# Kernel tuning notes

Hardware: AMD Instinct MI355X
Metric: run time of the kernel (lower is better)

Reference implementation:

```python
import jax, jax.numpy as jnp
import numpy as np

B, S, D, H, F = 8, 1024, 512, 8, 2048
EPS = 1e-3  # keras default for BatchNormalization and LayerNormalization


def _layernorm(x, g, b):
    m = jnp.mean(x, axis=-1, keepdims=True)
    v = jnp.var(x, axis=-1, keepdims=True)
    return (x - m) * jax.lax.rsqrt(v + EPS) * g + b


def setup_inputs() -> dict:
    key = jax.random.key(0)
    ks = jax.random.split(key, 16)
    sc = 0.02
    inp = {
        "Q": jax.random.normal(ks[0], (B, S, D), jnp.float32),
        "K": jax.random.normal(ks[1], (B, S, D), jnp.float32),
        "V": jax.random.normal(ks[2], (B, S, D), jnp.float32),
        # per-head QKV projections stacked: [H, D, D]
        "WQ": jax.random.normal(ks[3], (H, D, D), jnp.float32) * sc,
        "bQ": jnp.zeros((H, D), jnp.float32),
        "WK": jax.random.normal(ks[4], (H, D, D), jnp.float32) * sc,
        "bK": jnp.zeros((H, D), jnp.float32),
        "WV": jax.random.normal(ks[5], (H, D, D), jnp.float32) * sc,
        "bV": jnp.zeros((H, D), jnp.float32),
        "Wo": jax.random.normal(ks[6], (H * D, D), jnp.float32) * sc,
        "bo": jnp.zeros((D,), jnp.float32),
        # FeedForward
        "W0": jax.random.normal(ks[7], (D, F), jnp.float32) * sc,
        "b0": jnp.zeros((F,), jnp.float32),
        "g0": jnp.ones((F,), jnp.float32),
        "be0": jnp.zeros((F,), jnp.float32),
        "m0": jnp.zeros((F,), jnp.float32),   # BN moving mean
        "v0": jnp.ones((F,), jnp.float32),    # BN moving var
        "a0": jnp.zeros((S, F), jnp.float32),  # PReLU alpha (keras default shape/init)
        "W1": jax.random.normal(ks[8], (F, F), jnp.float32) * sc,
        "b1": jnp.zeros((F,), jnp.float32),
        "g1": jnp.ones((F,), jnp.float32),
        "be1": jnp.zeros((F,), jnp.float32),
        "m1": jnp.zeros((F,), jnp.float32),
        "v1": jnp.ones((F,), jnp.float32),
        "a1": jnp.zeros((S, F), jnp.float32),
        "W2": jax.random.normal(ks[9], (F, D), jnp.float32) * sc,
        "b2": jnp.zeros((D,), jnp.float32),
        "ln0g": jnp.ones((D,), jnp.float32),
        "ln0b": jnp.zeros((D,), jnp.float32),
        "ln1g": jnp.ones((D,), jnp.float32),
        "ln1b": jnp.zeros((D,), jnp.float32),
    }
    return inp


def reference(Q, K, V, WQ, bQ, WK, bK, WV, bV, Wo, bo,
              W0, b0, g0, be0, m0, v0, a0,
              W1, b1, g1, be1, m1, v1, a1,
              W2, b2, ln0g, ln0b, ln1g, ln1b):
    # ---- MultiHeadAttention (all heads batched) ----
    qh = jnp.einsum('bsd,hde->bhse', Q, WQ) + bQ[None, :, None, :]
    kh = jnp.einsum('bsd,hde->bhse', K, WK) + bK[None, :, None, :]
    vh = jnp.einsum('bsd,hde->bhse', V, WV) + bV[None, :, None, :]
    # NOTE: source scales by 1/dk, not 1/sqrt(dk)
    scores = jnp.einsum('bhse,bhte->bhst', qh, kh) * (1.0 / D)
    attn = jax.nn.softmax(scores, axis=-1)
    ctx = jnp.einsum('bhst,bhte->bhse', attn, vh)        # [B,H,S,D]
    cat = jnp.transpose(ctx, (0, 2, 1, 3)).reshape(B, S, H * D)
    mha = cat @ Wo + bo
    x = _layernorm(Q + mha, ln0g, ln0b)
    # ---- FeedForward (inference: BN uses moving stats, dropout off) ----
    h0 = x @ W0 + b0
    h0 = (h0 - m0) * jax.lax.rsqrt(v0 + EPS) * g0 + be0
    h0 = jnp.where(h0 > 0, h0, a0 * h0)                   # PReLU
    h1 = h0 @ W1 + b1
    h1 = (h1 - m1) * jax.lax.rsqrt(v1 + EPS) * g1 + be1
    h1 = jnp.where(h1 > 0, h1, a1 * h1)
    ff = h1 @ W2 + b2
    return _layernorm(x + ff, ln1g, ln1b)
```

## Files before the change

kernel.cpp:

```cpp
#include <hip/hip_runtime.h>
#include <hip/hip_bf16.h>
#include <cstdint>
#include <cstddef>

#define Sd 1024
#define Dd 512
#define Hd 8
#define Fd 2048
#define Bd 8
#define EPSf 1e-3f

typedef __bf16 bf16x8 __attribute__((ext_vector_type(8)));
typedef float f32x4 __attribute__((ext_vector_type(4)));
typedef __attribute__((address_space(3))) unsigned int lds_u32;
typedef __attribute__((address_space(1))) const unsigned int gl_u32;

#define BM 128
#define BN 128
#define BK 32

enum { EPI_BF16 = 0, EPI_F32 = 1, EPI_BNPRELU = 2, EPI_SCORES = 3, EPI_PV = 4 };

__device__ __forceinline__ void gl_lds16(const void* g, void* l) {
  __builtin_amdgcn_global_load_lds((gl_u32*)g, (lds_u32*)l, 16, 0, 0);
}


#define LGKM(n)                                                  \
  asm volatile("s_waitcnt lgkmcnt(" #n ")" ::: "memory");        \
  __builtin_amdgcn_sched_barrier(0)
#define VMC(n) asm volatile("s_waitcnt vmcnt(" #n ")" ::: "memory")

#define LDA_(dst, dof, xr, mh)                                               \
  _Pragma("unroll") for (int i_ = 0; i_ < 4; ++i_)                           \
      dst[i_] = *(const bf16x8*)(aw + (dof) + (xr) + (mh) * 8192 + i_ * 2048);
#define LDB_(dst, dof, xr)                                                   \
  _Pragma("unroll") for (int i_ = 0; i_ < 4; ++i_)                           \
      dst[i_] = *(const bf16x8*)(bw + (dof) + (xr) + i_ * 2048);
#define MFMAQ(q, av, bv)                                                     \
  __builtin_amdgcn_s_setprio(1);                                             \
  {                                                                          \
    _Pragma("unroll") for (int i_ = 0; i_ < 4; ++i_) {                       \
      _Pragma("unroll") for (int n_ = 0; n_ < 4; ++n_)                       \
          acc[(q) * 4 + i_][n_] = __builtin_amdgcn_mfma_f32_16x16x32_bf16(   \
              av[i_], bv[n_], acc[(q) * 4 + i_][n_], 0, 0, 0);               \
    }                                                                        \
  }                                                                          \
  __builtin_amdgcn_s_setprio(0)

template <int EPI>
__global__ __launch_bounds__(512, 2) void big_gemm(
    const __hip_bfloat16* __restrict__ A_,
    const __hip_bfloat16* __restrict__ B_,
    const float* __restrict__ bias_,
    void* __restrict__ C_, int ldc, int K,
    const float* __restrict__ bn_g, const float* __restrict__ bn_b,
    const float* __restrict__ bn_m, const float* __restrict__ bn_v,
    const float* __restrict__ pa) {
  __shared__ __align__(16) char lds[131072];
  const int tid = threadIdx.x;
  const int gx = gridDim.x;
  const int nwg = gx * gridDim.y;
  const int orig = blockIdx.y * gx + blockIdx.x;
  const int wgid = (orig & 7) * (nwg >> 3) + (orig >> 3);
  const int bx = wgid % gx;
  const int by = wgid / gx;
  const int m0 = by * 256, n0 = bx * 256;

  const int lane = tid & 63;
  const int wid = tid >> 6;
  const int wm = wid >> 2;
  const int wn = wid & 3;
  const int fr = lane & 15;
  const int kg = lane >> 4;

  const int r0 = tid >> 3;
  const int c0 = (tid & 7) ^ (r0 & 7);
  const size_t ldb = (size_t)K * 2;
  const char* Ab = (const char*)A_ + (size_t)(m0 + r0) * ldb + c0 * 16;
  const char* Bb = (const char*)B_ + (size_t)(n0 + r0) * ldb + c0 * 16;

  const int axor0 = (kg ^ (fr & 7)) << 4;
  const int axor1 = ((4 + kg) ^ (fr & 7)) << 4;
  const char* aw = lds + (wm << 14) + fr * 128;
  const char* bw = lds + 32768 + ((wn >> 1) << 14) + ((wn & 1) << 13) + fr * 128;

  auto STG = [&](int nof, int H, int u) {
    char* L = lds + nof + (H << 14) + tid * 16;
    const char* src = ((H < 2) ? Ab : Bb) + (size_t)((H & 1) * 128) * ldb + (size_t)u * 128;
    gl_lds16(src, L);
    gl_lds16(src + 64 * ldb, L + 8192);
  };

  bf16x8 aA[4], aB[4], bA[4], bB[4];
  f32x4 acc[8][4] = {};
  const int NT = K >> 6;

  STG(0, 0, 0); STG(0, 1, 0); STG(0, 2, 0); STG(0, 3, 0);
  STG(65536, 0, 1); STG(65536, 1, 1); STG(65536, 2, 1); STG(65536, 3, 1);
  VMC(8);
  __builtin_amdgcn_s_barrier();
  LDA_(aA, 0, axor0, 0);
  LDB_(bA, 0, axor0);

  for (int u = 0; u < NT; ++u) {
    const int dof = (u & 1) << 16;
    const int nof = dof ^ 65536;
    const bool stg = (u >= 1) & (u + 1 < NT);
    LDA_(aB, dof, axor0, 1);
    if (stg) { STG(nof, 0, u + 1); STG(nof, 1, u + 1); }
    LGKM(4);
    MFMAQ(0, aA, bA);
    LDA_(aA, dof, axor1, 0);
    LDB_(bB, dof, axor1);
    if (stg) { STG(nof, 2, u + 1); STG(nof, 3, u + 1); }
    LGKM(8);
    MFMAQ(1, aB, bA);
    LDA_(aB, dof, axor1, 1);
    LGKM(4);
    MFMAQ(0, aA, bB);
    LGKM(0);
    if (u + 1 < NT) {
      VMC(0);
      __builtin_amdgcn_s_barrier();
      LDA_(aA, nof, axor0, 0);
      LDB_(bA, nof, axor0);
    }
    MFMAQ(1, aB, bB);
  }

  char* C = (char*)C_;
#pragma unroll
  for (int ni = 0; ni < 4; ++ni) {
    const int col = n0 + wn * 64 + ni * 16 + fr;
    float bcol = 0.f, scale = 0.f, shift = 0.f;
    if (EPI != EPI_BF16) bcol = bias_[col];
    if (EPI == EPI_BNPRELU) {
      scale = bn_g[col] * rsqrtf(bn_v[col] + EPSf);
      shift = bn_b[col] - bn_m[col] * scale;
    }
#pragma unroll
    for (int mi = 0; mi < 8; ++mi) {
      const int rb = m0 + wm * 128 + mi * 16 + kg * 4;
#pragma unroll
      for (int j = 0; j < 4; ++j) {
        const int row = rb + j;
        float v = acc[mi][ni][j] + bcol;
        if (EPI == EPI_F32) {
          ((float*)C)[(size_t)row * ldc + col] = v;
        } else if (EPI == EPI_BF16) {
          ((__hip_bfloat16*)C)[(size_t)row * ldc + col] = __float2bfloat16(v);
        } else {
          v = v * scale + shift;
          const float aa = pa[(size_t)(row & (Sd - 1)) * Fd + col];
          v = v > 0.f ? v : aa * v;
          ((__hip_bfloat16*)C)[(size_t)row * ldc + col] = __float2bfloat16(v);
        }
      }
    }
  }
}

template <int EPI>
__global__ __launch_bounds__(256, 2) void bt_gemm(
    const __hip_bfloat16* __restrict__ A_, int lda, size_t sA1, size_t sA2,
    const __hip_bfloat16* __restrict__ B_, int ldb, size_t sB1, size_t sB2,
    const float* __restrict__ bias_, size_t sBi1, size_t sBi2,
    void* __restrict__ C_, int ldc, size_t sC1, size_t sC2,
    int K, float alpha, int zshift,
    const float* __restrict__ bn_g, const float* __restrict__ bn_b,
    const float* __restrict__ bn_m, const float* __restrict__ bn_v,
    const float* __restrict__ pa) {
  __shared__ __hip_bfloat16 As[BM * BK];
  __shared__ __hip_bfloat16 Bs[BN * BK];

  const int tid = threadIdx.x;
  const int z = blockIdx.z;
  const int z1 = z >> zshift;
  const int z2 = z & ((1 << zshift) - 1);
  const int m0 = blockIdx.y * BM;
  const int n0 = blockIdx.x * BN;

  const __hip_bfloat16* A = A_ + (size_t)z1 * sA1 + (size_t)z2 * sA2;
  const __hip_bfloat16* Bt = B_ + (size_t)z1 * sB1 + (size_t)z2 * sB2;
  const float* bi = bias_ ? bias_ + (size_t)z1 * sBi1 + (size_t)z2 * sBi2 : nullptr;

  const int lane = tid & 63;
  const int wv = tid >> 6;
  const int wm = (wv >> 1) * 64;
  const int wn = (wv & 1) * 64;
  const int fr = lane & 15;
  const int kg = lane >> 4;

  const int srow = tid >> 2, sch = tid & 3;
  const size_t ldab = (size_t)lda * 2, ldbb = (size_t)ldb * 2;
  const char* Ap = (const char*)A + (size_t)(m0 + srow) * ldab + sch * 16;
  const char* Ap2 = Ap + 64 * ldab;
  const char* Bp = (const char*)Bt + (size_t)(n0 + srow) * ldbb + sch * 16;
  const char* Bp2 = Bp + 64 * ldbb;
  char* lA = (char*)As + tid * 16;
  char* lB = (char*)Bs + tid * 16;

  f32x4 acc[4][4] = {};

  for (int kt = 0; kt < K; kt += BK) {
    const size_t kb = (size_t)kt * 2;
    gl_lds16(Ap + kb, lA);
    gl_lds16(Ap2 + kb, lA + 4096);
    gl_lds16(Bp + kb, lB);
    gl_lds16(Bp2 + kb, lB + 4096);
    __syncthreads();

    bf16x8 afr[4], bfr[4];
#pragma unroll
    for (int mi = 0; mi < 4; ++mi)
      afr[mi] = *reinterpret_cast<const bf16x8*>(As + (wm + mi * 16 + fr) * BK + kg * 8);
#pragma unroll
    for (int ni = 0; ni < 4; ++ni)
      bfr[ni] = *reinterpret_cast<const bf16x8*>(Bs + (wn + ni * 16 + fr) * BK + kg * 8);
#pragma unroll
    for (int mi = 0; mi < 4; ++mi)
#pragma unroll
      for (int ni = 0; ni < 4; ++ni)
        acc[mi][ni] = __builtin_amdgcn_mfma_f32_16x16x32_bf16(afr[mi], bfr[ni], acc[mi][ni], 0, 0, 0);
    __syncthreads();
  }

  char* C = (char*)C_ + ((size_t)z1 * sC1 + (size_t)z2 * sC2) * ((EPI == EPI_F32) ? 4 : 2);
  const float cs = (EPI == EPI_SCORES) ? bn_m[z2] : 0.f;
  float rp[4][4];
  if (EPI == EPI_SCORES) {
#pragma unroll
    for (int mi = 0; mi < 4; ++mi)
#pragma unroll
      for (int j = 0; j < 4; ++j) rp[mi][j] = 0.f;
  }
  float rinv_[4][4];
  if (EPI == EPI_PV) {
#pragma unroll
    for (int mi = 0; mi < 4; ++mi)
#pragma unroll
      for (int j = 0; j < 4; ++j)
        rinv_[mi][j] = 1.0f / bn_v[((size_t)z << 10) + m0 + wm + mi * 16 + kg * 4 + j];
  }
#pragma unroll
  for (int ni = 0; ni < 4; ++ni) {
    const int col = n0 + wn + ni * 16 + fr;
    float bcol = 0.f, scale = 0.f, shift = 0.f;
    if (bi) bcol = bi[col];
    if (EPI == EPI_BNPRELU) {
      scale = bn_g[col] * rsqrtf(bn_v[col] + EPSf);
      shift = bn_b[col] - bn_m[col] * scale;
    }
    const float wcol = (EPI == EPI_SCORES) ? bn_b[z2 * 8192 + z1 * 1024 + col] : 0.f;
#pragma unroll
    for (int mi = 0; mi < 4; ++mi) {
      const int rb = m0 + wm + mi * 16 + kg * 4;
#pragma unroll
      for (int j = 0; j < 4; ++j) {
        const int row = rb + j;
        if (EPI == EPI_SCORES) {
          const float e = __expf((acc[mi][ni][j] + bn_g[z2 * 8192 + z1 * 1024 + row] + wcol + cs) * alpha);
          rp[mi][j] += e;
          ((__hip_bfloat16*)C)[(size_t)row * ldc + col] = __float2bfloat16(e);
        } else if (EPI == EPI_PV) {
          ((__hip_bfloat16*)C)[(size_t)row * ldc + col] = __float2bfloat16(acc[mi][ni][j] * rinv_[mi][j]);
        } else {
          float v = acc[mi][ni][j] * alpha + bcol;
          if (EPI == EPI_F32) {
            ((float*)C)[(size_t)row * ldc + col] = v;
          } else if (EPI == EPI_BF16) {
            ((__hip_bfloat16*)C)[(size_t)row * ldc + col] = __float2bfloat16(v);
          } else {
            v = v * scale + shift;
            const float a = pa[(size_t)(row & (Sd - 1)) * Fd + col];
            v = v > 0.f ? v : a * v;
            ((__hip_bfloat16*)C)[(size_t)row * ldc + col] = __float2bfloat16(v);
          }
        }
      }
    }
  }
  if (EPI == EPI_SCORES) {
    float* rs = (float*)bn_v + ((size_t)z << 10) + m0 + wm;
#pragma unroll
    for (int mi = 0; mi < 4; ++mi)
#pragma unroll
      for (int j = 0; j < 4; ++j) {
        float v = rp[mi][j];
        v += __shfl_xor(v, 1);
        v += __shfl_xor(v, 2);
        v += __shfl_xor(v, 4);
        v += __shfl_xor(v, 8);
        if (fr == 0) atomicAdd(rs + mi * 16 + kg * 4 + j, v);
      }
  }
}

__global__ __launch_bounds__(256) void tconv(const float* __restrict__ src,
                                             __hip_bfloat16* __restrict__ dst,
                                             int N, int Kfull, size_t sIn, size_t sOut) {
  __shared__ __hip_bfloat16 t[64][65];
  const float* s = src + (size_t)blockIdx.z * sIn;
  __hip_bfloat16* d = dst + (size_t)blockIdx.z * sOut;
  const int k0 = blockIdx.y * 64, n0 = blockIdx.x * 64;
  const int tid = threadIdx.x;
#pragma unroll
  for (int i = 0; i < 4; ++i) {
    int slot = tid + i * 256;
    int r = slot >> 4, c = (slot & 15) * 4;
    const float4 v = *reinterpret_cast<const float4*>(s + (size_t)(k0 + r) * N + n0 + c);
    t[c + 0][r] = __float2bfloat16(v.x);
    t[c + 1][r] = __float2bfloat16(v.y);
    t[c + 2][r] = __float2bfloat16(v.z);
    t[c + 3][r] = __float2bfloat16(v.w);
  }
  __syncthreads();
#pragma unroll
  for (int i = 0; i < 2; ++i) {
    int slot = tid + i * 256;
    int n = slot >> 3, kc = (slot & 7) * 8;
    __hip_bfloat16 tmp[8];
#pragma unroll
    for (int j = 0; j < 8; ++j) tmp[j] = t[n][kc + j];
    *reinterpret_cast<float4*>(d + (size_t)(n0 + n) * Kfull + k0 + kc) =
        *reinterpret_cast<const float4*>(tmp);
  }
}

__global__ __launch_bounds__(256) void conv3(const float* __restrict__ s0, const float* __restrict__ s1,
                                             const float* __restrict__ s2,
                                             __hip_bfloat16* __restrict__ d0, __hip_bfloat16* __restrict__ d1,
                                             __hip_bfloat16* __restrict__ d2) {
  const float* s = blockIdx.y == 0 ? s0 : (blockIdx.y == 1 ? s1 : s2);
  __hip_bfloat16* d = blockIdx.y == 0 ? d0 : (blockIdx.y == 1 ? d1 : d2);
  const size_t i = (size_t)blockIdx.x * 256 + threadIdx.x;
  const float4 a = reinterpret_cast<const float4*>(s)[2 * i];
  const float4 b = reinterpret_cast<const float4*>(s)[2 * i + 1];
  __hip_bfloat16 tmp[8] = {
      __float2bfloat16(a.x), __float2bfloat16(a.y), __float2bfloat16(a.z), __float2bfloat16(a.w),
      __float2bfloat16(b.x), __float2bfloat16(b.y), __float2bfloat16(b.z), __float2bfloat16(b.w)};
  *reinterpret_cast<float4*>(d + 8 * i) = *reinterpret_cast<const float4*>(tmp);
}

__device__ inline float wave_max(float v) {
#pragma unroll
  for (int o = 32; o > 0; o >>= 1) v = fmaxf(v, __shfl_xor(v, o));
  return v;
}
__device__ inline float wave_sum(float v) {
#pragma unroll
  for (int o = 32; o > 0; o >>= 1) v += __shfl_xor(v, o);
  return v;
}

__device__ inline float b2f(unsigned short u) {
  unsigned x = ((unsigned)u) << 16; float f; __builtin_memcpy(&f, &x, 4); return f;
}

__global__ __launch_bounds__(256) void tvec(const float* __restrict__ WQ, const float* __restrict__ bK,
                                            const float* __restrict__ WK, const float* __restrict__ bQ,
                                            float* __restrict__ t1, float* __restrict__ t2) {
  const float* W = blockIdx.y == 0 ? WQ : WK;
  const float* bb = blockIdx.y == 0 ? bK : bQ;
  float* out = blockIdx.y == 0 ? t1 : t2;
  const int wv = threadIdx.x >> 6, lane = threadIdx.x & 63;
  const int hd = blockIdx.x * 4 + wv;
  const int h = hd >> 9;
  float acc = 0.f;
#pragma unroll
  for (int j = 0; j < 8; ++j) {
    const int e = lane + 64 * j;
    acc += W[(size_t)hd * 512 + e] * bb[h * 512 + e];
  }
  acc = wave_sum(acc);
  if (lane == 0) out[hd] = acc;
}

__global__ __launch_bounds__(256) void uw_kernel(const float* __restrict__ Q, const float* __restrict__ K,
                                                 const float* __restrict__ t1, const float* __restrict__ t2,
                                                 float* __restrict__ u, float* __restrict__ w) {
  const int tid = threadIdx.x;
  const size_t row = blockIdx.x;
  const float2 q = reinterpret_cast<const float2*>(Q + row * 512)[tid];
  const float2 k = reinterpret_cast<const float2*>(K + row * 512)[tid];
  const int c = tid * 2;
  __shared__ float redu[8][4], redw[8][4];
  const int wv = tid >> 6;
#pragma unroll
  for (int h = 0; h < 8; ++h) {
    float ua = q.x * t1[h * 512 + c] + q.y * t1[h * 512 + c + 1];
    float wa = k.x * t2[h * 512 + c] + k.y * t2[h * 512 + c + 1];
    ua = wave_sum(ua);
    wa = wave_sum(wa);
    if ((tid & 63) == 0) { redu[h][wv] = ua; redw[h][wv] = wa; }
  }
  __syncthreads();
  if (tid < 8)
    u[tid * 8192 + row] = redu[tid][0] + redu[tid][1] + redu[tid][2] + redu[tid][3];
  else if (tid < 16)
    w[(tid - 8) * 8192 + row] = redw[tid - 8][0] + redw[tid - 8][1] + redw[tid - 8][2] + redw[tid - 8][3];
}

__global__ __launch_bounds__(256) void cvec(const float* __restrict__ bQ, const float* __restrict__ bK,
                                            float* __restrict__ c) {
  const int h = blockIdx.x, tid = threadIdx.x;
  const float2 a = reinterpret_cast<const float2*>(bQ + h * 512)[tid];
  const float2 b = reinterpret_cast<const float2*>(bK + h * 512)[tid];
  float acc = wave_sum(a.x * b.x + a.y * b.y);
  __shared__ float red[4];
  if ((tid & 63) == 0) red[tid >> 6] = acc;
  __syncthreads();
  if (tid == 0) c[h] = red[0] + red[1] + red[2] + red[3];
}

__global__ __launch_bounds__(256) void bvo_kernel(const __hip_bfloat16* __restrict__ wot,
                                                  const float* __restrict__ bV,
                                                  const float* __restrict__ bo,
                                                  float* __restrict__ bvo) {
  const int wv = threadIdx.x >> 6, lane = threadIdx.x & 63;
  const int e = blockIdx.x * 4 + wv;
  float acc = 0.f;
#pragma unroll
  for (int j = 0; j < 64; ++j) {
    const int hd = lane + 64 * j;
    acc += b2f(*(const unsigned short*)&wot[(size_t)e * 4096 + hd]) * bV[hd];
  }
  acc = wave_sum(acc);
  if (lane == 0) bvo[e] = bo[e] + acc;
}

__global__ __launch_bounds__(256) void add_ln(const float* __restrict__ Xa, const float* __restrict__ Xb,
                                              const float* __restrict__ gamma, const float* __restrict__ beta,
                                              float* __restrict__ out, __hip_bfloat16* __restrict__ outb) {
  const int tid = threadIdx.x;
  const size_t base = (size_t)blockIdx.x * Dd;
  const float2 a = reinterpret_cast<const float2*>(Xa + base)[tid];
  const float2 b = reinterpret_cast<const float2*>(Xb + base)[tid];
  const float r0 = a.x + b.x, r1 = a.y + b.y;
  float s = wave_sum(r0 + r1);
  float q = wave_sum(r0 * r0 + r1 * r1);
  __shared__ float rs[4], rq[4];
  if ((tid & 63) == 0) { rs[tid >> 6] = s; rq[tid >> 6] = q; }
  __syncthreads();
  const float mean = (rs[0] + rs[1] + rs[2] + rs[3]) * (1.f / Dd);
  const float msq = (rq[0] + rq[1] + rq[2] + rq[3]) * (1.f / Dd);
  const float inv = rsqrtf(msq - mean * mean + EPSf);
  const int c = tid * 2;
  const float y0 = (r0 - mean) * inv * gamma[c] + beta[c];
  const float y1 = (r1 - mean) * inv * gamma[c + 1] + beta[c + 1];
  out[base + c] = y0;
  out[base + c + 1] = y1;
  if (outb) {
    outb[base + c] = __float2bfloat16(y0);
    outb[base + c + 1] = __float2bfloat16(y1);
  }
}

extern "C" void kernel_launch(void* const* d_in, const int* in_sizes, int n_in,
                              void* d_out, int out_size, void* d_ws, size_t ws_size,
                              hipStream_t stream) {
  const float* Q = (const float*)d_in[0];
  const float* K = (const float*)d_in[1];
  const float* V = (const float*)d_in[2];
  const float* WQ = (const float*)d_in[3];
  const float* bQ = (const float*)d_in[4];
  const float* WK = (const float*)d_in[5];
  const float* bK = (const float*)d_in[6];
  const float* WV = (const float*)d_in[7];
  const float* bV = (const float*)d_in[8];
  const float* Wo = (const float*)d_in[9];
  const float* bo = (const float*)d_in[10];
  const float* W0 = (const float*)d_in[11];
  const float* b0 = (const float*)d_in[12];
  const float* g0 = (const float*)d_in[13];
  const float* be0 = (const float*)d_in[14];
  const float* m0 = (const float*)d_in[15];
  const float* v0 = (const float*)d_in[16];
  const float* a0 = (const float*)d_in[17];
  const float* W1 = (const float*)d_in[18];
  const float* b1 = (const float*)d_in[19];
  const float* g1 = (const float*)d_in[20];
  const float* be1 = (const float*)d_in[21];
  const float* m1 = (const float*)d_in[22];
  const float* v1 = (const float*)d_in[23];
  const float* a1 = (const float*)d_in[24];
  const float* W2 = (const float*)d_in[25];
  const float* b2 = (const float*)d_in[26];
  const float* ln0g = (const float*)d_in[27];
  const float* ln0b = (const float*)d_in[28];
  const float* ln1g = (const float*)d_in[29];
  const float* ln1b = (const float*)d_in[30];

  typedef __hip_bfloat16 bf;
  const size_t MB = 1u << 20;
  const size_t KB = 1u << 10;
  char* ws = (char*)d_ws;
  bf* PR = (bf*)(ws);
  bf* wot = (bf*)(ws + 64 * MB);
  bf* wqbf = (bf*)(ws + 68 * MB);
  bf* wkbf = (bf*)(ws + 72 * MB);
  bf* wvbf = (bf*)(ws + 76 * MB);
  bf* wqkt = (bf*)(ws + 80 * MB);
  bf* sc = (bf*)(ws + 64 * MB);
  bf* kbf = (bf*)(ws + 96 * MB);
  bf* vbft = (bf*)(ws + 104 * MB);
  bf* qbf = (bf*)(ws + 112 * MB);
  bf* wvot = (bf*)(ws + 112 * MB);
  float* u = (float*)(ws + 116 * MB);
  float* w = (float*)(ws + 116 * MB + 256 * KB);
  float* rsum = (float*)(ws + 116 * MB + 512 * KB);
  float* t1 = (float*)(ws + 116 * MB + 768 * KB);
  float* t2 = (float*)(ws + 116 * MB + 784 * KB);
  float* cv = (float*)(ws + 116 * MB + 800 * KB);
  float* bvo = (float*)(ws + 116 * MB + 804 * KB);
  float* mha = (float*)(ws + 64 * MB);
  float* xbuf = (float*)(ws + 80 * MB);
  bf* xb = (bf*)(ws + 96 * MB);
  bf* w0t = (bf*)(ws + 104 * MB);
  bf* w1t = (bf*)(ws + 106 * MB);
  bf* w2t = (bf*)(ws + 114 * MB);
  bf* h0 = (bf*)(ws);
  bf* h1 = (bf*)(ws + 32 * MB);
  float* ff = (float*)(ws + 64 * MB);

  const size_t SD = (size_t)Sd * Dd;
  const size_t DD = (size_t)Dd * Dd;
  const size_t SS = (size_t)Sd * Sd;
  const size_t SDH = (size_t)Sd * Hd * Dd;
  const float* np = nullptr;

  conv3<<<dim3(2048, 2), 256, 0, stream>>>(Q, K, K, qbf, kbf, kbf);
  conv3<<<dim3(1024, 3), 256, 0, stream>>>(WQ, WK, WV, wqbf, wkbf, wvbf);
  tconv<<<dim3(8, 16, 8), 256, 0, stream>>>(V, vbft, Dd, Sd, SD, SD);
  tconv<<<dim3(8, 64, 1), 256, 0, stream>>>(Wo, wot, Dd, Hd * Dd, 0, 0);

  bt_gemm<EPI_BF16><<<dim3(4, 4, 8), 256, 0, stream>>>(
      wkbf, Dd, 0, DD, wqbf, Dd, 0, DD, np, 0, 0,
      wqkt, Dd, 0, DD, Dd, 1.f, 3, np, np, np, np, np);
  big_gemm<EPI_BF16><<<dim3(16, 32), 512, 0, stream>>>(
      qbf, wqkt, np, PR, Hd * Dd, Dd, np, np, np, np, np);

  bt_gemm<EPI_BF16><<<dim3(4, 4, 8), 256, 0, stream>>>(
      wot, Hd * Dd, 0, 512, wvbf, Dd, 0, DD, np, 0, 0,
      wvot, Hd * Dd, 0, 512, Dd, 1.f, 3, np, np, np, np, np);
  tvec<<<dim3(1024, 2), 256, 0, stream>>>(WQ, bK, WK, bQ, t1, t2);
  uw_kernel<<<Bd * Sd, 256, 0, stream>>>(Q, K, t1, t2, u, w);
  cvec<<<8, 256, 0, stream>>>(bQ, bK, cv);
  bvo_kernel<<<128, 256, 0, stream>>>(wot, bV, bo, bvo);
  hipMemsetAsync(rsum, 0, 64 * 1024 * sizeof(float), stream);

  for (int bp = 0; bp < 4; ++bp) {
    const bf* Ap = PR + (size_t)bp * 2 * SDH;
    bt_gemm<EPI_SCORES><<<dim3(8, 8, 16), 256, 0, stream>>>(
        Ap, Hd * Dd, SDH, 512, kbf + (size_t)bp * 2 * SD, Dd, SD, 0, np, 0, 0,
        sc, Sd, 8 * SS, SS, Dd, 1.f / (float)Dd, 3,
        u + bp * 2048, w + bp * 2048, cv, rsum + bp * 16384, np);
    bt_gemm<EPI_PV><<<dim3(4, 8, 16), 256, 0, stream>>>(
        sc, Sd, 8 * SS, SS, vbft + (size_t)bp * 2 * SD, Sd, SD, 0, np, 0, 0,
        (void*)Ap, Hd * Dd, SDH, 512, Sd, 1.f, 3,
        np, np, np, rsum + bp * 16384, np);
  }

  bt_gemm<EPI_F32><<<dim3(4, 64, 1), 256, 0, stream>>>(
      PR, Hd * Dd, 0, 0, wvot, Hd * Dd, 0, 0, bvo, 0, 0,
      mha, Dd, 0, 0, Hd * Dd, 1.f, 0, np, np, np, np, np);
  add_ln<<<Bd * Sd, 256, 0, stream>>>(Q, mha, ln0g, ln0b, xbuf, xb);

  tconv<<<dim3(32, 8, 1), 256, 0, stream>>>(W0, w0t, Fd, Dd, 0, 0);
  tconv<<<dim3(32, 32, 1), 256, 0, stream>>>(W1, w1t, Fd, Fd, 0, 0);
  tconv<<<dim3(8, 32, 1), 256, 0, stream>>>(W2, w2t, Dd, Fd, 0, 0);

  big_gemm<EPI_BNPRELU><<<dim3(8, 32), 512, 0, stream>>>(
      xb, w0t, b0, h0, Fd, Dd, g0, be0, m0, v0, a0);
  big_gemm<EPI_BNPRELU><<<dim3(8, 32), 512, 0, stream>>>(
      h0, w1t, b1, h1, Fd, Fd, g1, be1, m1, v1, a1);
  bt_gemm<EPI_F32><<<dim3(4, 64, 1), 256, 0, stream>>>(
      h1, Fd, 0, 0, w2t, Fd, 0, 0, b2, 0, 0,
      ff, Dd, 0, 0, Fd, 1.f, 0, np, np, np, np, np);
  add_ln<<<Bd * Sd, 256, 0, stream>>>(xbuf, ff, ln1g, ln1b, (float*)d_out, nullptr);
}
```

Baseline: 741.4 us.

## Move attention scores GEMM onto batched 256x256 pipelined big_gemm kernel

Generalizes big_gemm with separate A leading dimension, batch strides via blockIdx.z, an alpha scale and a fused exp/row-sum SCORES epilogue. The per-head QK^T scores GEMM moves from the simple 128x128 bt_gemm onto it, which has larger tiles, direct global-to-LDS loads and double buffering. The intent is better MFMA utilization and data reuse on the dominant attention GEMM. The trade-off is fewer workgroups per launch (256 instead of 1024) and a heavier epilogue that adds register pressure.

```diff
diff --git a/kernel.cpp b/kernel.cpp
--- a/kernel.cpp
+++ b/kernel.cpp
@@ -50,10 +50,10 @@
 
 template <int EPI>
 __global__ __launch_bounds__(512, 2) void big_gemm(
-    const __hip_bfloat16* __restrict__ A_,
-    const __hip_bfloat16* __restrict__ B_,
+    const __hip_bfloat16* __restrict__ A_, int lda, size_t sA1, size_t sA2,
+    const __hip_bfloat16* __restrict__ B_, size_t sB1,
     const float* __restrict__ bias_,
-    void* __restrict__ C_, int ldc, int K,
+    void* __restrict__ C_, int ldc, size_t sC, int K, float alpha,
     const float* __restrict__ bn_g, const float* __restrict__ bn_b,
     const float* __restrict__ bn_m, const float* __restrict__ bn_v,
     const float* __restrict__ pa) {
@@ -66,6 +66,8 @@
   const int bx = wgid % gx;
   const int by = wgid / gx;
   const int m0 = by * 256, n0 = bx * 256;
+  const int z = blockIdx.z;
+  const int z1 = z >> 3, z2 = z & 7;
 
   const int lane = tid & 63;
   const int wid = tid >> 6;
@@ -76,9 +78,11 @@
 
   const int r0 = tid >> 3;
   const int c0 = (tid & 7) ^ (r0 & 7);
-  const size_t ldb = (size_t)K * 2;
-  const char* Ab = (const char*)A_ + (size_t)(m0 + r0) * ldb + c0 * 16;
-  const char* Bb = (const char*)B_ + (size_t)(n0 + r0) * ldb + c0 * 16;
+  const size_t lda2 = (size_t)lda * 2;
+  const size_t ldb2 = (size_t)K * 2;
+  const char* Ab = (const char*)(A_ + (size_t)z1 * sA1 + (size_t)z2 * sA2) +
+                   (size_t)(m0 + r0) * lda2 + c0 * 16;
+  const char* Bb = (const char*)(B_ + (size_t)z1 * sB1) + (size_t)(n0 + r0) * ldb2 + c0 * 16;
 
   const int axor0 = (kg ^ (fr & 7)) << 4;
   const int axor1 = ((4 + kg) ^ (fr & 7)) << 4;
@@ -87,9 +91,10 @@
 
   auto STG = [&](int nof, int H, int u) {
     char* L = lds + nof + (H << 14) + tid * 16;
-    const char* src = ((H < 2) ? Ab : Bb) + (size_t)((H & 1) * 128) * ldb + (size_t)u * 128;
+    const size_t rs = (H < 2) ? lda2 : ldb2;
+    const char* src = ((H < 2) ? Ab : Bb) + (size_t)((H & 1) * 128) * rs + (size_t)u * 128;
     gl_lds16(src, L);
-    gl_lds16(src + 64 * ldb, L + 8192);
+    gl_lds16(src + 64 * rs, L + 8192);
   };
 
   bf16x8 aA[4], aB[4], bA[4], bB[4];
@@ -129,32 +134,67 @@
     MFMAQ(1, aB, bB);
   }
 
-  char* C = (char*)C_;
-#pragma unroll
-  for (int ni = 0; ni < 4; ++ni) {
-    const int col = n0 + wn * 64 + ni * 16 + fr;
-    float bcol = 0.f, scale = 0.f, shift = 0.f;
-    if (EPI != EPI_BF16) bcol = bias_[col];
-    if (EPI == EPI_BNPRELU) {
-      scale = bn_g[col] * rsqrtf(bn_v[col] + EPSf);
-      shift = bn_b[col] - bn_m[col] * scale;
-    }
+  char* C = (char*)C_ + (size_t)z * sC * ((EPI == EPI_F32) ? 4 : 2);
+  if (EPI == EPI_SCORES) {
+    const float cvv = bn_m[z2];
+    const float* ub = bn_g + (size_t)z2 * 8192 + (size_t)z1 * 1024;
+    const float* wb = bn_b + (size_t)z2 * 8192 + (size_t)z1 * 1024;
+    float* rs = (float*)bn_v + ((size_t)z << 10);
+    float wc[4];
+#pragma unroll
+    for (int ni = 0; ni < 4; ++ni) wc[ni] = wb[n0 + wn * 64 + ni * 16 + fr];
 #pragma unroll
     for (int mi = 0; mi < 8; ++mi) {
       const int rb = m0 + wm * 128 + mi * 16 + kg * 4;
+      float rowa[4] = {0.f, 0.f, 0.f, 0.f};
+#pragma unroll
+      for (int ni = 0; ni < 4; ++ni) {
+        const int col = n0 + wn * 64 + ni * 16 + fr;
+#pragma unroll
+        for (int j = 0; j < 4; ++j) {
+          const int row = rb + j;
+          const float e = __expf((acc[mi][ni][j] + ub[row] + wc[ni] + cvv) * alpha);
+          rowa[j] += e;
+          ((__hip_bfloat16*)C)[(size_t)row * ldc + col] = __float2bfloat16(e);
+        }
+      }
 #pragma unroll
       for (int j = 0; j < 4; ++j) {
-        const int row = rb + j;
-        float v = acc[mi][ni][j] + bcol;
-        if (EPI == EPI_F32) {
-          ((float*)C)[(size_t)row * ldc + col] = v;
-        } else if (EPI == EPI_BF16) {
-          ((__hip_bfloat16*)C)[(size_t)row * ldc + col] = __float2bfloat16(v);
-        } else {
-          v = v * scale + shift;
-          const float aa = pa[(size_t)(row & (Sd - 1)) * Fd + col];
-          v = v > 0.f ? v : aa * v;
-          ((__hip_bfloat16*)C)[(size_t)row * ldc + col] = __float2bfloat16(v);
+        float v = rowa[j];
+        v += __shfl_xor(v, 1);
+        v += __shfl_xor(v, 2);
+        v += __shfl_xor(v, 4);
+        v += __shfl_xor(v, 8);
+        if (fr == 0) atomicAdd(rs + rb + j, v);
+      }
+    }
+  } else {
+#pragma unroll
+    for (int ni = 0; ni < 4; ++ni) {
+      const int col = n0 + wn * 64 + ni * 16 + fr;
+      float bcol = 0.f, scale = 0.f, shift = 0.f;
+      if (EPI != EPI_BF16) bcol = bias_[col];
+      if (EPI == EPI_BNPRELU) {
+        scale = bn_g[col] * rsqrtf(bn_v[col] + EPSf);
+        shift = bn_b[col] - bn_m[col] * scale;
+      }
+#pragma unroll
+      for (int mi = 0; mi < 8; ++mi) {
+        const int rb = m0 + wm * 128 + mi * 16 + kg * 4;
+#pragma unroll
+        for (int j = 0; j < 4; ++j) {
+          const int row = rb + j;
+          float v = acc[mi][ni][j] * alpha + bcol;
+          if (EPI == EPI_F32) {
+            ((float*)C)[(size_t)row * ldc + col] = v;
+          } else if (EPI == EPI_BF16) {
+            ((__hip_bfloat16*)C)[(size_t)row * ldc + col] = __float2bfloat16(v);
+          } else {
+            v = v * scale + shift;
+            const float aa = pa[(size_t)(row & (Sd - 1)) * Fd + col];
+            v = v > 0.f ? v : aa * v;
+            ((__hip_bfloat16*)C)[(size_t)row * ldc + col] = __float2bfloat16(v);
+          }
         }
       }
     }
@@ -227,14 +267,6 @@
   }
 
   char* C = (char*)C_ + ((size_t)z1 * sC1 + (size_t)z2 * sC2) * ((EPI == EPI_F32) ? 4 : 2);
-  const float cs = (EPI == EPI_SCORES) ? bn_m[z2] : 0.f;
-  float rp[4][4];
-  if (EPI == EPI_SCORES) {
-#pragma unroll
-    for (int mi = 0; mi < 4; ++mi)
-#pragma unroll
-      for (int j = 0; j < 4; ++j) rp[mi][j] = 0.f;
-  }
   float rinv_[4][4];
   if (EPI == EPI_PV) {
 #pragma unroll
@@ -252,18 +284,13 @@
       scale = bn_g[col] * rsqrtf(bn_v[col] + EPSf);
       shift = bn_b[col] - bn_m[col] * scale;
     }
-    const float wcol = (EPI == EPI_SCORES) ? bn_b[z2 * 8192 + z1 * 1024 + col] : 0.f;
 #pragma unroll
     for (int mi = 0; mi < 4; ++mi) {
       const int rb = m0 + wm + mi * 16 + kg * 4;
 #pragma unroll
       for (int j = 0; j < 4; ++j) {
         const int row = rb + j;
-        if (EPI == EPI_SCORES) {
-          const float e = __expf((acc[mi][ni][j] + bn_g[z2 * 8192 + z1 * 1024 + row] + wcol + cs) * alpha);
-          rp[mi][j] += e;
-          ((__hip_bfloat16*)C)[(size_t)row * ldc + col] = __float2bfloat16(e);
-        } else if (EPI == EPI_PV) {
+        if (EPI == EPI_PV) {
           ((__hip_bfloat16*)C)[(size_t)row * ldc + col] = __float2bfloat16(acc[mi][ni][j] * rinv_[mi][j]);
         } else {
           float v = acc[mi][ni][j] * alpha + bcol;
@@ -280,20 +307,6 @@
         }
       }
     }
-  }
-  if (EPI == EPI_SCORES) {
-    float* rs = (float*)bn_v + ((size_t)z << 10) + m0 + wm;
-#pragma unroll
-    for (int mi = 0; mi < 4; ++mi)
-#pragma unroll
-      for (int j = 0; j < 4; ++j) {
-        float v = rp[mi][j];
-        v += __shfl_xor(v, 1);
-        v += __shfl_xor(v, 2);
-        v += __shfl_xor(v, 4);
-        v += __shfl_xor(v, 8);
-        if (fr == 0) atomicAdd(rs + mi * 16 + kg * 4 + j, v);
-      }
   }
 }
 
@@ -538,8 +551,8 @@
   bt_gemm<EPI_BF16><<<dim3(4, 4, 8), 256, 0, stream>>>(
       wkbf, Dd, 0, DD, wqbf, Dd, 0, DD, np, 0, 0,
       wqkt, Dd, 0, DD, Dd, 1.f, 3, np, np, np, np, np);
-  big_gemm<EPI_BF16><<<dim3(16, 32), 512, 0, stream>>>(
-      qbf, wqkt, np, PR, Hd * Dd, Dd, np, np, np, np, np);
+  big_gemm<EPI_BF16><<<dim3(16, 32, 1), 512, 0, stream>>>(
+      qbf, Dd, 0, 0, wqkt, 0, np, PR, Hd * Dd, 0, Dd, 1.f, np, np, np, np, np);
 
   bt_gemm<EPI_BF16><<<dim3(4, 4, 8), 256, 0, stream>>>(
       wot, Hd * Dd, 0, 512, wvbf, Dd, 0, DD, np, 0, 0,
@@ -552,9 +565,9 @@
 
   for (int bp = 0; bp < 4; ++bp) {
     const bf* Ap = PR + (size_t)bp * 2 * SDH;
-    bt_gemm<EPI_SCORES><<<dim3(8, 8, 16), 256, 0, stream>>>(
-        Ap, Hd * Dd, SDH, 512, kbf + (size_t)bp * 2 * SD, Dd, SD, 0, np, 0, 0,
-        sc, Sd, 8 * SS, SS, Dd, 1.f / (float)Dd, 3,
+    big_gemm<EPI_SCORES><<<dim3(4, 4, 16), 512, 0, stream>>>(
+        Ap, Hd * Dd, SDH, 512, kbf + (size_t)bp * 2 * SD, SD, np,
+        sc, Sd, SS, Dd, 1.f / (float)Dd,
         u + bp * 2048, w + bp * 2048, cv, rsum + bp * 16384, np);
     bt_gemm<EPI_PV><<<dim3(4, 8, 16), 256, 0, stream>>>(
         sc, Sd, 8 * SS, SS, vbft + (size_t)bp * 2 * SD, Sd, SD, 0, np, 0, 0,
@@ -571,10 +584,10 @@
   tconv<<<dim3(32, 32, 1), 256, 0, stream>>>(W1, w1t, Fd, Fd, 0, 0);
   tconv<<<dim3(8, 32, 1), 256, 0, stream>>>(W2, w2t, Dd, Fd, 0, 0);
 
-  big_gemm<EPI_BNPRELU><<<dim3(8, 32), 512, 0, stream>>>(
-      xb, w0t, b0, h0, Fd, Dd, g0, be0, m0, v0, a0);
-  big_gemm<EPI_BNPRELU><<<dim3(8, 32), 512, 0, stream>>>(
-      h0, w1t, b1, h1, Fd, Fd, g1, be1, m1, v1, a1);
+  big_gemm<EPI_BNPRELU><<<dim3(8, 32, 1), 512, 0, stream>>>(
+      xb, Dd, 0, 0, w0t, 0, b0, h0, Fd, 0, Dd, 1.f, g0, be0, m0, v0, a0);
+  big_gemm<EPI_BNPRELU><<<dim3(8, 32, 1), 512, 0, stream>>>(
+      h0, Fd, 0, 0, w1t, 0, b1, h1, Fd, 0, Fd, 1.f, g1, be1, m1, v1, a1);
   bt_gemm<EPI_F32><<<dim3(4, 64, 1), 256, 0, stream>>>(
       h1, Fd, 0, 0, w2t, Fd, 0, 0, b2, 0, 0,
       ff, Dd, 0, 0, Fd, 1.f, 0, np, np, np, np, np);
```

Result: faster. 698.7 us (-5.8%).
